# Kernel optimization log

Hardware: AMD Instinct MI355X
Metric: run time of the kernel (lower is better)

## Reference

```python
import jax, jax.numpy as jnp
import numpy as np

N_NODES = 100000
N_EDGES = 600000
HID = 128
N_ETYPES = 8


def setup_inputs() -> dict:
    key = jax.random.key(0)
    ks = jax.random.split(key, 10)
    s = 1.0 / np.sqrt(HID)
    return {
        "h": jax.random.normal(ks[0], (N_NODES, HID), dtype=jnp.float32),
        "edge_index": jax.random.randint(ks[1], (2, N_EDGES), 0, N_NODES, dtype=jnp.int64),
        "edge_type": jax.random.randint(ks[2], (N_EDGES,), 0, N_ETYPES, dtype=jnp.int64),
        # per-edge-type Linear(hidden, hidden): weight (T, H_out, H_in) stored as (T, H_in, H_out) for einsum
        "message_W": jax.random.uniform(ks[3], (N_ETYPES, HID, HID), jnp.float32, -s, s),
        "message_b": jax.random.uniform(ks[4], (N_ETYPES, HID), jnp.float32, -s, s),
        # GRUCell params (torch layout): w_ih (3H, H), w_hh (3H, H), b_ih (3H,), b_hh (3H,)
        "gru_w_ih": jax.random.uniform(ks[5], (3 * HID, HID), jnp.float32, -s, s),
        "gru_w_hh": jax.random.uniform(ks[6], (3 * HID, HID), jnp.float32, -s, s),
        "gru_b_ih": jax.random.uniform(ks[7], (3 * HID,), jnp.float32, -s, s),
        "gru_b_hh": jax.random.uniform(ks[8], (3 * HID,), jnp.float32, -s, s),
    }


def reference(h, edge_index, edge_type, message_W, message_b,
              gru_w_ih, gru_w_hh, gru_b_ih, gru_b_hh):
    num_nodes = h.shape[0]
    src, dst = edge_index[0], edge_index[1]

    # Transform every node by every edge-type Linear once: (N, T, H).
    # Equivalent to per-type msg = h[src] @ W[t].T + b[t] gathered by edge type.
    all_msgs = jnp.einsum('nh,thd->ntd', h, message_W) + message_b  # (N, T, H)
    msg = all_msgs[src, edge_type]                                   # (E, H) gather
    messages = jax.ops.segment_sum(msg, dst, num_segments=num_nodes)  # scatter-add

    # GRUCell: r,z,n gates (torch semantics)
    gi = messages @ gru_w_ih.T + gru_b_ih  # (N, 3H)
    gh = h @ gru_w_hh.T + gru_b_hh         # (N, 3H)
    i_r, i_z, i_n = jnp.split(gi, 3, axis=-1)
    h_r, h_z, h_n = jnp.split(gh, 3, axis=-1)
    r = jax.nn.sigmoid(i_r + h_r)
    z = jax.nn.sigmoid(i_z + h_z)
    n = jnp.tanh(i_n + r * h_n)
    return (1.0 - z) * n + z * h
```

## Files before the change

kernel.cpp:

```cpp
#include <hip/hip_runtime.h>

#define HID 128
#define NTY 8

typedef __attribute__((ext_vector_type(8))) short bf16x8;
typedef __attribute__((ext_vector_type(4))) float f32x4;

__device__ __forceinline__ unsigned short f2bf(float x) {
    unsigned u = __float_as_uint(x);
    u += 0x7FFF + ((u >> 16) & 1);
    return (unsigned short)(u >> 16);
}
__device__ __forceinline__ float bf2f(unsigned short s) {
    return __uint_as_float(((unsigned)s) << 16);
}
__device__ __forceinline__ float sigmoidf_fast(float x) {
    return 1.f / (1.f + __expf(-x));
}
__device__ __forceinline__ float tanhf_fast(float x) {
    return 1.f - 2.f / (1.f + __expf(2.f * x));
}

__global__ void conv_all_kernel(const float* __restrict__ h, unsigned short* __restrict__ hbf, int nh,
                                const float* __restrict__ W, unsigned short* __restrict__ wfr,
                                const float* __restrict__ wih, const float* __restrict__ whh,
                                unsigned short* __restrict__ wpkf,
                                int* __restrict__ sortedT, int capE,
                                int* __restrict__ deg, int N, int* __restrict__ tcnt)
{
    int i = blockIdx.x * 256 + threadIdx.x;
    if (i < nh) { hbf[i] = f2bf(h[i]); return; }
    i -= nh;
    if (i < 131072) {
        int e = i & 7, lane = (i >> 3) & 63, cb = (i >> 9) & 7, kc = (i >> 12) & 3, t = i >> 14;
        int lr = lane & 15, quad = lane >> 4;
        int d = cb * 16 + lr;
        int k = kc * 32 + quad * 8 + e;
        wfr[i] = f2bf(W[(t << 14) + (k << 7) + d]);
        return;
    }
    i -= 131072;
    if (i < 98304) {
        int e = i & 7, lane = (i >> 3) & 63, f = i >> 9;
        int ct = f & 7, fg = f >> 3;
        int g3 = fg % 3, kc = fg / 3;
        int lr = lane & 15, quad = lane >> 4;
        int d = ct * 16 + lr;
        int kk = quad * 8 + e;
        float v;
        if (kc < 4) v = wih[(g3 * 128 + d) * 128 + kc * 32 + kk];
        else        v = whh[(g3 * 128 + d) * 128 + (kc - 4) * 32 + kk];
        wpkf[i] = f2bf(v);
        return;
    }
    i -= 98304;
    if (i < capE) { sortedT[i] = -1; return; }
    i -= capE;
    if (i < N) { deg[i] = 0; return; }
    i -= N;
    if (i < NTY) tcnt[i] = 0;
}

__global__ void hist_kernel(const int* __restrict__ etype, const int* __restrict__ ei,
                            int E, int* __restrict__ tcnt, int* __restrict__ deg) {
    __shared__ int lc[NTY];
    if (threadIdx.x < NTY) lc[threadIdx.x] = 0;
    __syncthreads();
    int stride = gridDim.x * blockDim.x;
    for (int i = blockIdx.x * blockDim.x + threadIdx.x; i < E; i += stride) {
        atomicAdd(&lc[etype[i]], 1);
        if (deg) atomicAdd(&deg[ei[E + i]], 1);
    }
    __syncthreads();
    if (threadIdx.x < NTY) atomicAdd(&tcnt[threadIdx.x], lc[threadIdx.x]);
}

__global__ void scanA_kernel(const int* __restrict__ deg, int* __restrict__ start,
                             int* __restrict__ bsum, int N) {
    __shared__ int s[256];
    int i = blockIdx.x * 256 + threadIdx.x;
    int v = (i < N) ? deg[i] : 0;
    s[threadIdx.x] = v;
    __syncthreads();
    for (int off = 1; off < 256; off <<= 1) {
        int t = (threadIdx.x >= off) ? s[threadIdx.x - off] : 0;
        __syncthreads();
        s[threadIdx.x] += t;
        __syncthreads();
    }
    if (i < N) start[i] = s[threadIdx.x] - v;
    if (threadIdx.x == 255) bsum[blockIdx.x] = s[255];
}

__global__ void scanB_kernel(int* __restrict__ bsum, int nb,
                             const int* __restrict__ tcnt, int* __restrict__ tcur) {
    __shared__ int s[512];
    int tx = threadIdx.x;
    int v = (tx < nb) ? bsum[tx] : 0;
    s[tx] = v;
    __syncthreads();
    for (int off = 1; off < 512; off <<= 1) {
        int t = (tx >= off) ? s[tx - off] : 0;
        __syncthreads();
        s[tx] += t;
        __syncthreads();
    }
    if (tx < nb) bsum[tx] = s[tx] - v;
    if (tx == 0) {
        int off = 0;
        for (int t = 0; t < NTY; ++t) { tcur[t] = off; off += (tcnt[t] + 127) & ~127; }
    }
}

__global__ void scanC_kernel(int* __restrict__ start, const int* __restrict__ bsum,
                             int* __restrict__ dcur, int N, int E) {
    int i = blockIdx.x * 256 + threadIdx.x;
    if (i < N) {
        int v = start[i] + bsum[blockIdx.x];
        start[i] = v;
        dcur[i] = v;
    }
    if (i == 0) start[N] = E;
}

__global__ __launch_bounds__(256) void scatter_agg(
    const int* __restrict__ etype, const int* __restrict__ ei, int E,
    int* __restrict__ tcur, int* __restrict__ dcur,
    int* __restrict__ sortedT, int* __restrict__ q, int mode)
{
    __shared__ int lcnt[NTY];
    __shared__ int lbase[NTY];
    int tx = threadIdx.x;
    int chunk = (E + gridDim.x - 1) / gridDim.x;
    int s = blockIdx.x * chunk;
    int e = s + chunk; if (e > E) e = E;
    if (tx < NTY) lcnt[tx] = 0;
    __syncthreads();
    for (int i = s + tx; i < e; i += 256)
        atomicAdd(&lcnt[etype[i]], 1);
    __syncthreads();
    if (tx < NTY) {
        lbase[tx] = atomicAdd(&tcur[tx], lcnt[tx]);
        lcnt[tx] = 0;
    }
    __syncthreads();
    for (int i = s + tx; i < e; i += 256) {
        int t = etype[i];
        int lp = atomicAdd(&lcnt[t], 1);
        sortedT[lbase[t] + lp] = i;
        if (mode) q[i] = atomicAdd(&dcur[ei[E + i]], 1);
    }
}

__global__ __launch_bounds__(256) void msg_gemm(
    const unsigned short* __restrict__ hbf, const int* __restrict__ ei, int E,
    const int* __restrict__ etype, const unsigned short* __restrict__ wfr,
    const float* __restrict__ bias, const int* __restrict__ sortedT,
    const int* __restrict__ q, unsigned short* __restrict__ M,
    float* __restrict__ msum, int mode)
{
    __shared__ unsigned short hs[128][136];
    __shared__ int srcs[128], aux[128];
    __shared__ int stype;

    int tx = threadIdx.x;
    int base = blockIdx.x * 128;
    if (tx < 128) {
        int id = sortedT[base + tx];
        srcs[tx] = (id >= 0) ? ei[id] : -1;
        aux[tx]  = (id >= 0) ? (mode ? ei[E + id] : q[id]) : -1;
    }
    if (tx == 0) { int id0 = sortedT[base]; stype = (id0 >= 0) ? etype[id0] : -1; }
    __syncthreads();
    int t = stype;
    if (t < 0) return;

    for (int f = tx; f < 2048; f += 256) {
        int row = f >> 4, c8 = (f & 15) * 8;
        int s = srcs[row]; if (s < 0) s = 0;
        *(uint4*)&hs[row][c8] = *(const uint4*)&hbf[(size_t)s * 128 + c8];
    }
    __syncthreads();

    int lane = tx & 63, w = tx >> 6;
    int r0 = (w >> 1) * 64, c0 = (w & 1) * 64;
    int lr = lane & 15, quad = lane >> 4;
    f32x4 acc[4][4] = {};

    const unsigned short* wt = wfr + (t << 14) + ((unsigned)(c0 >> 4) << 9) + (lane << 3);
    #pragma unroll
    for (int kc = 0; kc < 4; ++kc) {
        bf16x8 af[4], wf[4];
        #pragma unroll
        for (int rb = 0; rb < 4; ++rb) af[rb] = *(const bf16x8*)&hs[r0 + rb * 16 + lr][kc * 32 + quad * 8];
        #pragma unroll
        for (int cb = 0; cb < 4; ++cb) wf[cb] = *(const bf16x8*)&wt[(kc << 12) + (cb << 9)];
        #pragma unroll
        for (int rb = 0; rb < 4; ++rb)
            #pragma unroll
            for (int cb = 0; cb < 4; ++cb)
                acc[rb][cb] = __builtin_amdgcn_mfma_f32_16x16x32_bf16(wf[cb], af[rb], acc[rb][cb], 0, 0, 0);
    }

    float4 bv4[4];
    #pragma unroll
    for (int cb = 0; cb < 4; ++cb)
        bv4[cb] = *(const float4*)&bias[t * 128 + c0 + cb * 16 + quad * 4];

    #pragma unroll
    for (int rb = 0; rb < 4; ++rb) {
        int e = r0 + rb * 16 + lr;
        int mr = aux[e];
        if (mr < 0) continue;
        #pragma unroll
        for (int cb = 0; cb < 4; ++cb) {
            int d0 = c0 + cb * 16 + quad * 4;
            f32x4 a = acc[rb][cb];
            if (mode) {
                atomicAdd(&msum[(size_t)mr * 128 + d0 + 0], a[0] + bv4[cb].x);
                atomicAdd(&msum[(size_t)mr * 128 + d0 + 1], a[1] + bv4[cb].y);
                atomicAdd(&msum[(size_t)mr * 128 + d0 + 2], a[2] + bv4[cb].z);
                atomicAdd(&msum[(size_t)mr * 128 + d0 + 3], a[3] + bv4[cb].w);
            } else {
                uint2 v;
                v.x = (unsigned)f2bf(a[0] + bv4[cb].x) | ((unsigned)f2bf(a[1] + bv4[cb].y) << 16);
                v.y = (unsigned)f2bf(a[2] + bv4[cb].z) | ((unsigned)f2bf(a[3] + bv4[cb].w) << 16);
                *(uint2*)&M[(size_t)mr * 128 + d0] = v;
            }
        }
    }
}

__global__ __launch_bounds__(512, 4) void gru_fused(
    const unsigned short* __restrict__ M, const int* __restrict__ start,
    const float* __restrict__ msum_fb, const unsigned short* __restrict__ hbf,
    const unsigned short* __restrict__ wpkf, const float* __restrict__ bih,
    const float* __restrict__ bhh, const float* __restrict__ hf,
    float* __restrict__ out, int N, int mode)
{
    __shared__ unsigned short As[4][2048];
    __shared__ int bnds_l[65];

    int tx = threadIdx.x;
    int n0 = blockIdx.x * 64;

    if (tx <= 64) {
        int idx = n0 + tx; if (idx > N) idx = N;
        bnds_l[tx] = (mode == 0) ? start[idx] : 0;
    }

    int lane = tx & 63, w = tx >> 6;
    int lr = lane & 15, quad = lane >> 4;
    int rt = w & 3, cg = w >> 2;
    int node = n0 + rt * 16 + lr;
    bool valid = node < N;
    int nc = valid ? node : (N - 1);

    bf16x8 afh[4];
    {
        const unsigned short* hrow = hbf + ((size_t)nc << 7) + (quad << 3);
        #pragma unroll
        for (int k4 = 0; k4 < 4; ++k4) afh[k4] = *(const bf16x8*)&hrow[k4 * 32];
    }
    __syncthreads();

    {
        int ln = tx >> 3, j8 = tx & 7;
        float a[16];
        #pragma unroll
        for (int j = 0; j < 16; ++j) a[j] = 0.f;

        if (mode == 0) {
            int rs = bnds_l[ln], re = bnds_l[ln + 1];
            uint4 c0v, c1v;
            if (rs < re) {
                const unsigned short* p = M + (size_t)rs * 128 + j8 * 16;
                c0v = *(const uint4*)p;
                c1v = *(const uint4*)(p + 8);
            }
            for (int r = rs; r < re; ++r) {
                uint4 p0 = c0v, p1 = c1v;
                if (r + 1 < re) {
                    const unsigned short* pn = M + (size_t)(r + 1) * 128 + j8 * 16;
                    c0v = *(const uint4*)pn;
                    c1v = *(const uint4*)(pn + 8);
                }
                const unsigned short* q0 = (const unsigned short*)&p0;
                const unsigned short* q1 = (const unsigned short*)&p1;
                #pragma unroll
                for (int u = 0; u < 8; ++u) {
                    a[u]     += bf2f(q0[u]);
                    a[8 + u] += bf2f(q1[u]);
                }
            }
        } else {
            int n = n0 + ln; int nc2 = (n < N) ? n : N - 1;
            #pragma unroll
            for (int j = 0; j < 4; ++j) {
                float4 v = *(const float4*)&msum_fb[(size_t)nc2 * 128 + j8 * 16 + j * 4];
                a[j * 4 + 0] = v.x; a[j * 4 + 1] = v.y; a[j * 4 + 2] = v.z; a[j * 4 + 3] = v.w;
            }
        }

        unsigned short tmp[16];
        #pragma unroll
        for (int j = 0; j < 16; ++j) tmp[j] = f2bf(a[j]);
        int lrw = ln & 15, wv = ln >> 4;
        int swz = (lrw & 7) << 4;
        int b0 = ((lrw << 8) + (j8 << 5)) ^ swz;
        int b1 = ((lrw << 8) + (j8 << 5) + 16) ^ swz;
        *(uint4*)((char*)&As[wv][0] + b0) = *(const uint4*)&tmp[0];
        *(uint4*)((char*)&As[wv][0] + b1) = *(const uint4*)&tmp[8];
    }
    __syncthreads();

    const unsigned short* AsW = &As[rt][0];
    const unsigned short* wg = wpkf + (lane << 3);

    f32x4 aR[4] = {}, aZ[4] = {}, aI[4] = {}, aH[4] = {};
    #pragma unroll
    for (int kc = 0; kc < 8; ++kc) {
        bf16x8 af;
        if (kc < 4) {
            int byte = ((lr << 8) + (kc << 6) + (quad << 4)) ^ ((lr & 7) << 4);
            af = *(const bf16x8*)((char*)AsW + byte);
        } else {
            af = afh[kc - 4];
        }
        #pragma unroll
        for (int g3 = 0; g3 < 3; ++g3) {
            #pragma unroll
            for (int ct = 0; ct < 4; ++ct) {
                bf16x8 wf = *(const bf16x8*)&wg[(unsigned)((kc * 3 + g3) * 8 + cg * 4 + ct) << 9];
                if (g3 == 0)      aR[ct] = __builtin_amdgcn_mfma_f32_16x16x32_bf16(wf, af, aR[ct], 0, 0, 0);
                else if (g3 == 1) aZ[ct] = __builtin_amdgcn_mfma_f32_16x16x32_bf16(wf, af, aZ[ct], 0, 0, 0);
                else if (kc < 4)  aI[ct] = __builtin_amdgcn_mfma_f32_16x16x32_bf16(wf, af, aI[ct], 0, 0, 0);
                else              aH[ct] = __builtin_amdgcn_mfma_f32_16x16x32_bf16(wf, af, aH[ct], 0, 0, 0);
            }
        }
    }

    if (valid) {
        #pragma unroll
        for (int ct = 0; ct < 4; ++ct) {
            int d0 = cg * 64 + ct * 16 + quad * 4;
            f32x4 bir = *(const f32x4*)&bih[d0],       bhr = *(const f32x4*)&bhh[d0];
            f32x4 biz = *(const f32x4*)&bih[128 + d0], bhz = *(const f32x4*)&bhh[128 + d0];
            f32x4 bin = *(const f32x4*)&bih[256 + d0], bhn = *(const f32x4*)&bhh[256 + d0];
            f32x4 h0 = *(const f32x4*)&hf[(size_t)node * 128 + d0];
            f32x4 o;
            #pragma unroll
            for (int j = 0; j < 4; ++j) {
                float r  = sigmoidf_fast(aR[ct][j] + bir[j] + bhr[j]);
                float z  = sigmoidf_fast(aZ[ct][j] + biz[j] + bhz[j]);
                float nn = tanhf_fast(aI[ct][j] + bin[j] + r * (aH[ct][j] + bhn[j]));
                o[j] = (1.f - z) * nn + z * h0[j];
            }
            *(f32x4*)&out[(size_t)node * 128 + d0] = o;
        }
    }
}

extern "C" void kernel_launch(void* const* d_in, const int* in_sizes, int n_in,
                              void* d_out, int out_size, void* d_ws, size_t ws_size,
                              hipStream_t stream)
{
    const float* h     = (const float*)d_in[0];
    const int*   ei    = (const int*)d_in[1];
    const int*   etype = (const int*)d_in[2];
    const float* W     = (const float*)d_in[3];
    const float* b     = (const float*)d_in[4];
    const float* wih   = (const float*)d_in[5];
    const float* whh   = (const float*)d_in[6];
    const float* bih   = (const float*)d_in[7];
    const float* bhh   = (const float*)d_in[8];
    float* out = (float*)d_out;

    int E = in_sizes[1] / 2;
    int N = in_sizes[0] / HID;
    int capE = ((E + 127) / 128 + NTY) * 128;
    int nbA = (N + 255) / 256;

    char* p = (char*)d_ws;
    auto alloc = [&](size_t bytes) { char* r = p; p += (bytes + 255) & ~(size_t)255; return r; };
    unsigned short* hbf  = (unsigned short*)alloc((size_t)N * 128 * 2);
    unsigned short* wfr  = (unsigned short*)alloc((size_t)131072 * 2);
    unsigned short* wpkf = (unsigned short*)alloc((size_t)98304 * 2);
    int* tcnt    = (int*)alloc(NTY * 4);
    int* tcur    = (int*)alloc(NTY * 4);
    int* sortedT = (int*)alloc((size_t)capE * 4);
    unsigned short* M = (unsigned short*)alloc((size_t)E * 128 * 2);
    int* q     = (int*)alloc((size_t)E * 4);
    int* deg   = (int*)alloc((size_t)N * 4);
    int* start = (int*)alloc((size_t)(N + 1) * 4);
    int* dcur  = (int*)alloc((size_t)N * 4);
    int* bsum  = (int*)alloc(512 * 4);
    int mode = ((size_t)(p - (char*)d_ws) <= ws_size) ? 0 : 1;

    if (mode == 1) hipMemsetAsync(out, 0, (size_t)N * 128 * 4, stream);

    int totalConv = N * 128 + 131072 + 98304 + capE + N + NTY;
    conv_all_kernel<<<(totalConv + 255) / 256, 256, 0, stream>>>(
        h, hbf, N * 128, W, wfr, wih, whh, wpkf, sortedT, capE, deg, N, tcnt);

    hist_kernel<<<1024, 256, 0, stream>>>(etype, ei, E, tcnt, (mode == 0) ? deg : nullptr);
    if (mode == 0)
        scanA_kernel<<<nbA, 256, 0, stream>>>(deg, start, bsum, N);
    scanB_kernel<<<1, 512, 0, stream>>>(bsum, nbA, tcnt, tcur);
    if (mode == 0)
        scanC_kernel<<<nbA, 256, 0, stream>>>(start, bsum, dcur, N, E);
    scatter_agg<<<256, 256, 0, stream>>>(etype, ei, E, tcur, dcur, sortedT, q, (mode == 0) ? 1 : 0);

    msg_gemm<<<capE / 128, 256, 0, stream>>>(hbf, ei, E, etype, wfr, b, sortedT, q, M, out, mode);
    gru_fused<<<(N + 63) / 64, 512, 0, stream>>>(M, start, out, hbf, wpkf, bih, bhh, h, out, N, mode);
}
```

Baseline: 385.0 us.

## Sort edges by (type, dst) with one counting sort and drop fallback mode

Replaces the separate per-type bucketing and per-destination CSR with a single counting sort keyed by (edge type, destination), using a histogram over 8*N bins, a three-stage scan with 128-padding per type, and one scatter pass. The message GEMM now writes its outputs contiguously in sorted order, so the aux/q indirection goes away. The GRU kernel walks eight per-type segments per node to sum messages. The atomic fallback mode is removed. This costs a larger histogram/scan over 800k entries, a serial bsum scan, and more complex segment walking in gru_fused, and it assumes the workspace is always large enough.

```diff
diff --git a/kernel.cpp b/kernel.cpp
--- a/kernel.cpp
+++ b/kernel.cpp
@@ -25,8 +25,8 @@
                                 const float* __restrict__ W, unsigned short* __restrict__ wfr,
                                 const float* __restrict__ wih, const float* __restrict__ whh,
                                 unsigned short* __restrict__ wpkf,
-                                int* __restrict__ sortedT, int capE,
-                                int* __restrict__ deg, int N, int* __restrict__ tcnt)
+                                int* __restrict__ sortedE, int capE,
+                                int* __restrict__ seg8, int M8)
 {
     int i = blockIdx.x * 256 + threadIdx.x;
     if (i < nh) { hbf[i] = f2bf(h[i]); return; }
@@ -54,32 +54,22 @@
         return;
     }
     i -= 98304;
-    if (i < capE) { sortedT[i] = -1; return; }
+    if (i < capE) { sortedE[i] = -1; return; }
     i -= capE;
-    if (i < N) { deg[i] = 0; return; }
-    i -= N;
-    if (i < NTY) tcnt[i] = 0;
-}
-
-__global__ void hist_kernel(const int* __restrict__ etype, const int* __restrict__ ei,
-                            int E, int* __restrict__ tcnt, int* __restrict__ deg) {
-    __shared__ int lc[NTY];
-    if (threadIdx.x < NTY) lc[threadIdx.x] = 0;
-    __syncthreads();
+    if (i < M8) seg8[i] = 0;
+}
+
+__global__ void hist8_kernel(const int* __restrict__ etype, const int* __restrict__ ei,
+                             int E, int N, int* __restrict__ seg8) {
     int stride = gridDim.x * blockDim.x;
-    for (int i = blockIdx.x * blockDim.x + threadIdx.x; i < E; i += stride) {
-        atomicAdd(&lc[etype[i]], 1);
-        if (deg) atomicAdd(&deg[ei[E + i]], 1);
-    }
-    __syncthreads();
-    if (threadIdx.x < NTY) atomicAdd(&tcnt[threadIdx.x], lc[threadIdx.x]);
-}
-
-__global__ void scanA_kernel(const int* __restrict__ deg, int* __restrict__ start,
-                             int* __restrict__ bsum, int N) {
+    for (int i = blockIdx.x * blockDim.x + threadIdx.x; i < E; i += stride)
+        atomicAdd(&seg8[etype[i] * N + ei[E + i]], 1);
+}
+
+__global__ void scanA_kernel(int* __restrict__ seg8, int* __restrict__ bsum, int M8) {
     __shared__ int s[256];
     int i = blockIdx.x * 256 + threadIdx.x;
-    int v = (i < N) ? deg[i] : 0;
+    int v = (i < M8) ? seg8[i] : 0;
     s[threadIdx.x] = v;
     __syncthreads();
     for (int off = 1; off < 256; off <<= 1) {
@@ -88,89 +78,82 @@
         s[threadIdx.x] += t;
         __syncthreads();
     }
-    if (i < N) start[i] = s[threadIdx.x] - v;
+    if (i < M8) seg8[i] = s[threadIdx.x] - v;
     if (threadIdx.x == 255) bsum[blockIdx.x] = s[255];
 }
 
-__global__ void scanB_kernel(int* __restrict__ bsum, int nb,
-                             const int* __restrict__ tcnt, int* __restrict__ tcur) {
-    __shared__ int s[512];
+__global__ void scanBbig_kernel(int* __restrict__ bsum, int nb,
+                                const int* __restrict__ seg8, int N, int E,
+                                int* __restrict__ padB, int* __restrict__ padA) {
+    __shared__ int s[256];
     int tx = threadIdx.x;
-    int v = (tx < nb) ? bsum[tx] : 0;
-    s[tx] = v;
-    __syncthreads();
-    for (int off = 1; off < 512; off <<= 1) {
+    int C = (nb + 255) / 256;
+    int lo = tx * C, hi = lo + C; if (hi > nb) hi = nb;
+    int sum = 0;
+    for (int j = lo; j < hi; ++j) sum += bsum[j];
+    s[tx] = sum;
+    __syncthreads();
+    for (int off = 1; off < 256; off <<= 1) {
         int t = (tx >= off) ? s[tx - off] : 0;
         __syncthreads();
         s[tx] += t;
         __syncthreads();
     }
-    if (tx < nb) bsum[tx] = s[tx] - v;
+    int run = s[tx] - sum;
+    for (int j = lo; j < hi; ++j) { int v = bsum[j]; bsum[j] = run; run += v; }
+    __syncthreads();
     if (tx == 0) {
-        int off = 0;
-        for (int t = 0; t < NTY; ++t) { tcur[t] = off; off += (tcnt[t] + 127) & ~127; }
-    }
-}
-
-__global__ void scanC_kernel(int* __restrict__ start, const int* __restrict__ bsum,
-                             int* __restrict__ dcur, int N, int E) {
+        int r[9];
+        for (int t = 0; t < 8; ++t) { int k = t * N; r[t] = seg8[k] + bsum[k >> 8]; }
+        r[8] = E;
+        int pb = 0;
+        for (int t = 0; t < 8; ++t) {
+            padB[t] = pb;
+            padA[t] = pb - r[t];
+            int c = r[t + 1] - r[t];
+            pb += (c + 127) & ~127;
+        }
+        padB[8] = pb;
+    }
+}
+
+__global__ void scanC_kernel(int* __restrict__ seg8, const int* __restrict__ bsum,
+                             const int* __restrict__ padA, int M8, int N) {
     int i = blockIdx.x * 256 + threadIdx.x;
-    if (i < N) {
-        int v = start[i] + bsum[blockIdx.x];
-        start[i] = v;
-        dcur[i] = v;
-    }
-    if (i == 0) start[N] = E;
-}
-
-__global__ __launch_bounds__(256) void scatter_agg(
-    const int* __restrict__ etype, const int* __restrict__ ei, int E,
-    int* __restrict__ tcur, int* __restrict__ dcur,
-    int* __restrict__ sortedT, int* __restrict__ q, int mode)
-{
-    __shared__ int lcnt[NTY];
-    __shared__ int lbase[NTY];
-    int tx = threadIdx.x;
-    int chunk = (E + gridDim.x - 1) / gridDim.x;
-    int s = blockIdx.x * chunk;
-    int e = s + chunk; if (e > E) e = E;
-    if (tx < NTY) lcnt[tx] = 0;
-    __syncthreads();
-    for (int i = s + tx; i < e; i += 256)
-        atomicAdd(&lcnt[etype[i]], 1);
-    __syncthreads();
-    if (tx < NTY) {
-        lbase[tx] = atomicAdd(&tcur[tx], lcnt[tx]);
-        lcnt[tx] = 0;
-    }
-    __syncthreads();
-    for (int i = s + tx; i < e; i += 256) {
-        int t = etype[i];
-        int lp = atomicAdd(&lcnt[t], 1);
-        sortedT[lbase[t] + lp] = i;
-        if (mode) q[i] = atomicAdd(&dcur[ei[E + i]], 1);
+    if (i < M8) {
+        int t = i / N;
+        seg8[i] += bsum[i >> 8] + padA[t];
+    }
+}
+
+__global__ void scatter8_kernel(const int* __restrict__ etype, const int* __restrict__ ei,
+                                int E, int N, int* __restrict__ seg8, int* __restrict__ sortedE) {
+    int stride = gridDim.x * blockDim.x;
+    for (int i = blockIdx.x * blockDim.x + threadIdx.x; i < E; i += stride) {
+        int pos = atomicAdd(&seg8[etype[i] * N + ei[E + i]], 1);
+        sortedE[pos] = ei[i];
     }
 }
 
 __global__ __launch_bounds__(256) void msg_gemm(
-    const unsigned short* __restrict__ hbf, const int* __restrict__ ei, int E,
-    const int* __restrict__ etype, const unsigned short* __restrict__ wfr,
-    const float* __restrict__ bias, const int* __restrict__ sortedT,
-    const int* __restrict__ q, unsigned short* __restrict__ M,
-    float* __restrict__ msum, int mode)
+    const unsigned short* __restrict__ hbf, const unsigned short* __restrict__ wfr,
+    const float* __restrict__ bias, const int* __restrict__ sortedE,
+    const int* __restrict__ padB, unsigned short* __restrict__ M)
 {
     __shared__ unsigned short hs[128][136];
-    __shared__ int srcs[128], aux[128];
+    __shared__ int srcs[128];
     __shared__ int stype;
 
     int tx = threadIdx.x;
     int base = blockIdx.x * 128;
-    if (tx < 128) {
-        int id = sortedT[base + tx];
-        srcs[tx] = (id >= 0) ? ei[id] : -1;
-        aux[tx]  = (id >= 0) ? (mode ? ei[E + id] : q[id]) : -1;
-    }
-    if (tx == 0) { int id0 = sortedT[base]; stype = (id0 >= 0) ? etype[id0] : -1; }
+    if (tx < 128) srcs[tx] = sortedE[base + tx];
+    if (tx == 0) {
+        int t = -1;
+        #pragma unroll
+        for (int tt = 0; tt < 8; ++tt)
+            if (base >= padB[tt] && base < padB[tt + 1]) t = tt;
+        stype = t;
+    }
     __syncthreads();
     int t = stype;
     if (t < 0) return;
@@ -210,43 +193,42 @@
     #pragma unroll
     for (int rb = 0; rb < 4; ++rb) {
         int e = r0 + rb * 16 + lr;
-        int mr = aux[e];
-        if (mr < 0) continue;
+        size_t mrow = (size_t)(base + e);
         #pragma unroll
         for (int cb = 0; cb < 4; ++cb) {
             int d0 = c0 + cb * 16 + quad * 4;
             f32x4 a = acc[rb][cb];
-            if (mode) {
-                atomicAdd(&msum[(size_t)mr * 128 + d0 + 0], a[0] + bv4[cb].x);
-                atomicAdd(&msum[(size_t)mr * 128 + d0 + 1], a[1] + bv4[cb].y);
-                atomicAdd(&msum[(size_t)mr * 128 + d0 + 2], a[2] + bv4[cb].z);
-                atomicAdd(&msum[(size_t)mr * 128 + d0 + 3], a[3] + bv4[cb].w);
-            } else {
-                uint2 v;
-                v.x = (unsigned)f2bf(a[0] + bv4[cb].x) | ((unsigned)f2bf(a[1] + bv4[cb].y) << 16);
-                v.y = (unsigned)f2bf(a[2] + bv4[cb].z) | ((unsigned)f2bf(a[3] + bv4[cb].w) << 16);
-                *(uint2*)&M[(size_t)mr * 128 + d0] = v;
-            }
+            uint2 v;
+            v.x = (unsigned)f2bf(a[0] + bv4[cb].x) | ((unsigned)f2bf(a[1] + bv4[cb].y) << 16);
+            v.y = (unsigned)f2bf(a[2] + bv4[cb].z) | ((unsigned)f2bf(a[3] + bv4[cb].w) << 16);
+            *(uint2*)&M[mrow * 128 + d0] = v;
         }
     }
 }
 
 __global__ __launch_bounds__(512, 4) void gru_fused(
-    const unsigned short* __restrict__ M, const int* __restrict__ start,
-    const float* __restrict__ msum_fb, const unsigned short* __restrict__ hbf,
+    const unsigned short* __restrict__ M, const int* __restrict__ segE,
+    const int* __restrict__ padB, const unsigned short* __restrict__ hbf,
     const unsigned short* __restrict__ wpkf, const float* __restrict__ bih,
     const float* __restrict__ bhh, const float* __restrict__ hf,
-    float* __restrict__ out, int N, int mode)
+    float* __restrict__ out, int N)
 {
     __shared__ unsigned short As[4][2048];
-    __shared__ int bnds_l[65];
+    __shared__ int bnds_l[520];
 
     int tx = threadIdx.x;
     int n0 = blockIdx.x * 64;
 
-    if (tx <= 64) {
-        int idx = n0 + tx; if (idx > N) idx = N;
-        bnds_l[tx] = (mode == 0) ? start[idx] : 0;
+    for (int jl = tx; jl < 520; jl += 512) {
+        int t = jl / 65, j = jl - t * 65;
+        int nidx = n0 + j - 1;
+        int v;
+        if (nidx < 0) v = padB[t];
+        else {
+            if (nidx > N - 1) nidx = N - 1;
+            v = segE[t * N + nidx];
+        }
+        bnds_l[jl] = v;
     }
 
     int lane = tx & 63, w = tx >> 6;
@@ -270,36 +252,42 @@
         #pragma unroll
         for (int j = 0; j < 16; ++j) a[j] = 0.f;
 
-        if (mode == 0) {
-            int rs = bnds_l[ln], re = bnds_l[ln + 1];
-            uint4 c0v, c1v;
-            if (rs < re) {
-                const unsigned short* p = M + (size_t)rs * 128 + j8 * 16;
+        int tcur = 0;
+        int r = bnds_l[ln], re = bnds_l[ln + 1];
+        while (r >= re && tcur < 7) {
+            ++tcur;
+            r = bnds_l[tcur * 65 + ln];
+            re = bnds_l[tcur * 65 + ln + 1];
+        }
+        bool have = (r < re);
+        uint4 c0v, c1v;
+        if (have) {
+            const unsigned short* p = M + (size_t)r * 128 + j8 * 16;
+            c0v = *(const uint4*)p;
+            c1v = *(const uint4*)(p + 8);
+        }
+        while (have) {
+            uint4 p0 = c0v, p1 = c1v;
+            int rn = r + 1, tn = tcur, ren = re;
+            while (rn >= ren && tn < 7) {
+                ++tn;
+                rn = bnds_l[tn * 65 + ln];
+                ren = bnds_l[tn * 65 + ln + 1];
+            }
+            bool haveN = (rn < ren);
+            if (haveN) {
+                const unsigned short* p = M + (size_t)rn * 128 + j8 * 16;
                 c0v = *(const uint4*)p;
                 c1v = *(const uint4*)(p + 8);
             }
-            for (int r = rs; r < re; ++r) {
-                uint4 p0 = c0v, p1 = c1v;
-                if (r + 1 < re) {
-                    const unsigned short* pn = M + (size_t)(r + 1) * 128 + j8 * 16;
-                    c0v = *(const uint4*)pn;
-                    c1v = *(const uint4*)(pn + 8);
-                }
-                const unsigned short* q0 = (const unsigned short*)&p0;
-                const unsigned short* q1 = (const unsigned short*)&p1;
-                #pragma unroll
-                for (int u = 0; u < 8; ++u) {
-                    a[u]     += bf2f(q0[u]);
-                    a[8 + u] += bf2f(q1[u]);
-                }
-            }
-        } else {
-            int n = n0 + ln; int nc2 = (n < N) ? n : N - 1;
+            const unsigned short* q0 = (const unsigned short*)&p0;
+            const unsigned short* q1 = (const unsigned short*)&p1;
             #pragma unroll
-            for (int j = 0; j < 4; ++j) {
-                float4 v = *(const float4*)&msum_fb[(size_t)nc2 * 128 + j8 * 16 + j * 4];
-                a[j * 4 + 0] = v.x; a[j * 4 + 1] = v.y; a[j * 4 + 2] = v.z; a[j * 4 + 3] = v.w;
-            }
+            for (int u = 0; u < 8; ++u) {
+                a[u]     += bf2f(q0[u]);
+                a[8 + u] += bf2f(q1[u]);
+            }
+            r = rn; tcur = tn; re = ren; have = haveN;
         }
 
         unsigned short tmp[16];
@@ -378,39 +366,33 @@
 
     int E = in_sizes[1] / 2;
     int N = in_sizes[0] / HID;
+    int M8 = N * 8;
+    int nbA = (M8 + 255) / 256;
     int capE = ((E + 127) / 128 + NTY) * 128;
-    int nbA = (N + 255) / 256;
 
     char* p = (char*)d_ws;
     auto alloc = [&](size_t bytes) { char* r = p; p += (bytes + 255) & ~(size_t)255; return r; };
     unsigned short* hbf  = (unsigned short*)alloc((size_t)N * 128 * 2);
     unsigned short* wfr  = (unsigned short*)alloc((size_t)131072 * 2);
     unsigned short* wpkf = (unsigned short*)alloc((size_t)98304 * 2);
-    int* tcnt    = (int*)alloc(NTY * 4);
-    int* tcur    = (int*)alloc(NTY * 4);
-    int* sortedT = (int*)alloc((size_t)capE * 4);
-    unsigned short* M = (unsigned short*)alloc((size_t)E * 128 * 2);
-    int* q     = (int*)alloc((size_t)E * 4);
-    int* deg   = (int*)alloc((size_t)N * 4);
-    int* start = (int*)alloc((size_t)(N + 1) * 4);
-    int* dcur  = (int*)alloc((size_t)N * 4);
-    int* bsum  = (int*)alloc(512 * 4);
-    int mode = ((size_t)(p - (char*)d_ws) <= ws_size) ? 0 : 1;
-
-    if (mode == 1) hipMemsetAsync(out, 0, (size_t)N * 128 * 4, stream);
-
-    int totalConv = N * 128 + 131072 + 98304 + capE + N + NTY;
+    int* seg8    = (int*)alloc((size_t)M8 * 4);
+    int* bsum    = (int*)alloc((size_t)nbA * 4);
+    int* sortedE = (int*)alloc((size_t)capE * 4);
+    int* padB    = (int*)alloc(9 * 4);
+    int* padA    = (int*)alloc(8 * 4);
+    unsigned short* M = (unsigned short*)alloc((size_t)capE * 128 * 2);
+    (void)ws_size;
+
+    int totalConv = N * 128 + 131072 + 98304 + capE + M8;
     conv_all_kernel<<<(totalConv + 255) / 256, 256, 0, stream>>>(
-        h, hbf, N * 128, W, wfr, wih, whh, wpkf, sortedT, capE, deg, N, tcnt);
-
-    hist_kernel<<<1024, 256, 0, stream>>>(etype, ei, E, tcnt, (mode == 0) ? deg : nullptr);
-    if (mode == 0)
-        scanA_kernel<<<nbA, 256, 0, stream>>>(deg, start, bsum, N);
-    scanB_kernel<<<1, 512, 0, stream>>>(bsum, nbA, tcnt, tcur);
-    if (mode == 0)
-        scanC_kernel<<<nbA, 256, 0, stream>>>(start, bsum, dcur, N, E);
-    scatter_agg<<<256, 256, 0, stream>>>(etype, ei, E, tcur, dcur, sortedT, q, (mode == 0) ? 1 : 0);
-
-    msg_gemm<<<capE / 128, 256, 0, stream>>>(hbf, ei, E, etype, wfr, b, sortedT, q, M, out, mode);
-    gru_fused<<<(N + 63) / 64, 512, 0, stream>>>(M, start, out, hbf, wpkf, bih, bhh, h, out, N, mode);
-}
+        h, hbf, N * 128, W, wfr, wih, whh, wpkf, sortedE, capE, seg8, M8);
+
+    hist8_kernel<<<1024, 256, 0, stream>>>(etype, ei, E, N, seg8);
+    scanA_kernel<<<nbA, 256, 0, stream>>>(seg8, bsum, M8);
+    scanBbig_kernel<<<1, 256, 0, stream>>>(bsum, nbA, seg8, N, E, padB, padA);
+    scanC_kernel<<<nbA, 256, 0, stream>>>(seg8, bsum, padA, M8, N);
+    scatter8_kernel<<<1024, 256, 0, stream>>>(etype, ei, E, N, seg8, sortedE);
+
+    msg_gemm<<<capE / 128, 256, 0, stream>>>(hbf, wfr, b, sortedE, padB, M);
+    gru_fused<<<(N + 63) / 64, 512, 0, stream>>>(M, seg8, padB, hbf, wpkf, bih, bhh, h, out, N);
+}
```

Result: no change. 380.8 us (-1.1%).
